# Kernel tuning notes

Hardware: AMD Instinct MI355X
Metric: run time of the kernel (lower is better)

The kernel has to match this reference:

```python
import jax, jax.numpy as jnp
import numpy as np

N_NODES = 50000
N_EDGES = 800000
IN_F = 128
HID = 128
N_REL = 8


def setup_inputs() -> dict:
    key = jax.random.key(0)
    ks = jax.random.split(key, 12)
    s = 0.05
    return {
        "in_feat": jax.random.normal(ks[0], (N_NODES, IN_F), dtype=jnp.float32),
        "W1": jax.random.normal(ks[1], (N_REL, IN_F, HID), dtype=jnp.float32) * s,
        "W1_self": jax.random.normal(ks[2], (IN_F, HID), dtype=jnp.float32) * s,
        "b1": jnp.zeros((HID,), dtype=jnp.float32),
        "W2": jax.random.normal(ks[3], (N_REL, HID, HID), dtype=jnp.float32) * s,
        "W2_self": jax.random.normal(ks[4], (HID, HID), dtype=jnp.float32) * s,
        "b2": jnp.zeros((HID,), dtype=jnp.float32),
        "fc_w": jax.random.normal(ks[5], (HID, 1), dtype=jnp.float32) * s,
        "fc_b": jnp.zeros((1,), dtype=jnp.float32),
        "src": jax.random.randint(ks[6], (N_EDGES,), 0, N_NODES),
        "dst": jax.random.randint(ks[7], (N_EDGES,), 0, N_NODES),
        "etypes": jax.random.randint(ks[8], (N_EDGES,), 0, N_REL),
    }


def _rel_graph_conv(h, W, W_self, b, src, dst, etypes, n_nodes):
    # Transform node features once per relation: [R, N, H]
    xr = jnp.einsum('nd,rdh->rnh', h, W)
    # Per-edge message: gather relation-specific transformed source features [E, H]
    msgs = xr[etypes, src]
    # Scatter-sum aggregation to destination nodes [N, H]
    agg = jax.ops.segment_sum(msgs, dst, num_segments=n_nodes)
    # Self-loop + bias + ReLU (DGL RelGraphConv defaults)
    return jax.nn.relu(agg + h @ W_self + b)


def reference(in_feat, W1, W1_self, b1, W2, W2_self, b2, fc_w, fc_b, src, dst, etypes):
    n = in_feat.shape[0]
    h = _rel_graph_conv(in_feat, W1, W1_self, b1, src, dst, etypes, n)
    # dropout layers are identity in eval mode
    h = _rel_graph_conv(h, W2, W2_self, b2, src, dst, etypes, n)
    pooled = jnp.mean(h, axis=0, keepdims=True)  # AvgPooling over one graph -> [1, H]
    logits = pooled @ fc_w + fc_b                # [1, 1]
    return jax.nn.sigmoid(logits)
```

## Files before the change

kernel.cpp:

```cpp
#include <hip/hip_runtime.h>

#define NNODES 50000
#define NEDGES 800000
#define F 128
#define NREL 8
#define NOUT 1152
#define NBKT 98
#define BSH 9
#define SEG 16384
#define NTILES 391
#define GEMM_BLOCKS (8 * 9 * 49)
#define CSR_BLOCKS 196

typedef float f32x4 __attribute__((ext_vector_type(4)));
typedef float f32x2 __attribute__((ext_vector_type(2)));

typedef __attribute__((address_space(3))) void lds_void;
typedef const __attribute__((address_space(1))) void glb_void;
__device__ __forceinline__ void gll16(const void* g, void* l) {
  __builtin_amdgcn_global_load_lds(
      (glb_void*)(unsigned long long)g,
      (lds_void*)(unsigned)(unsigned long long)l, 16, 0, 0);
}

#define PREP_ZERO  33
#define PREP_CVT   6250
#define PREP_W     144
__global__ __launch_bounds__(256)
void k_prep(const float* __restrict__ in_feat, unsigned* __restrict__ feat0,
            const float* __restrict__ W1, const float* __restrict__ W1s,
            unsigned* __restrict__ Wt1,
            const float* __restrict__ W2, const float* __restrict__ W2s,
            unsigned* __restrict__ Wt2,
            float* __restrict__ pooled_p, int* __restrict__ bcur) {
  const int b = blockIdx.x, t = threadIdx.x;
  if (b < 32) {
    pooled_p[b * 256 + t] = 0.f;
  } else if (b < PREP_ZERO) {
    if (t <= NBKT) bcur[t] = 0;
  } else if (b < PREP_ZERO + PREP_CVT) {
    int i = (b - PREP_ZERO) * 256 + t;
    float4 v = ((const float4*)in_feat)[i];
    unsigned pk = 0;
    pk = __builtin_amdgcn_cvt_pk_fp8_f32(v.x, v.y, pk, false);
    pk = __builtin_amdgcn_cvt_pk_fp8_f32(v.z, v.w, pk, true);
    feat0[i] = pk;
  } else {
    int w2 = (b >= PREP_ZERO + PREP_CVT + PREP_W);
    int idx = (b - PREP_ZERO - PREP_CVT - (w2 ? PREP_W : 0)) * 256 + t;
    int n = idx >> 5, k0 = (idx & 31) * 4;
    int r = n >> 7, c = n & 127;
    const float* Wr = w2 ? W2 : W1;
    const float* Ws = w2 ? W2s : W1s;
    float v0, v1, v2, v3;
    if (r < NREL) {
      v0 = Wr[((size_t)(r * F + k0 + 0)) * F + c];
      v1 = Wr[((size_t)(r * F + k0 + 1)) * F + c];
      v2 = Wr[((size_t)(r * F + k0 + 2)) * F + c];
      v3 = Wr[((size_t)(r * F + k0 + 3)) * F + c];
    } else {
      v0 = Ws[(size_t)(k0 + 0) * F + c];
      v1 = Ws[(size_t)(k0 + 1) * F + c];
      v2 = Ws[(size_t)(k0 + 2) * F + c];
      v3 = Ws[(size_t)(k0 + 3) * F + c];
    }
    unsigned pk = 0;
    pk = __builtin_amdgcn_cvt_pk_fp8_f32(v0, v1, pk, false);
    pk = __builtin_amdgcn_cvt_pk_fp8_f32(v2, v3, pk, true);
    (w2 ? Wt2 : Wt1)[idx] = pk;
  }
}

__global__ __launch_bounds__(512)
void k_fsort(const int* __restrict__ ebuf, const int* __restrict__ bcur,
             int* __restrict__ rowptr, int* __restrict__ edata) {
  __shared__ int cnt[512];
  __shared__ int pos[512];
  __shared__ int ws2[512];
  __shared__ int bc_s;
  const int b = blockIdx.x, t = threadIdx.x;
  int myc = (t < NBKT) ? bcur[t] : 0;
  ws2[t] = (t < b) ? myc : 0;
  if (t == b) bc_s = myc;
  __syncthreads();
  for (int off = 1; off < 512; off <<= 1) {
    int x = (t >= off) ? ws2[t - off] : 0;
    __syncthreads();
    ws2[t] += x;
    __syncthreads();
  }
  const int beg = ws2[511];
  const int cntb = bc_s;
  const int sbeg = b * SEG;

  cnt[t] = 0;
  __syncthreads();
  for (int e = t; e < cntb; e += 512)
    atomicAdd(&cnt[((unsigned)ebuf[sbeg + e]) >> 19], 1);
  __syncthreads();
  int myn = cnt[t];
  ws2[t] = myn;
  __syncthreads();
  for (int off = 1; off < 512; off <<= 1) {
    int x = (t >= off) ? ws2[t - off] : 0;
    __syncthreads();
    ws2[t] += x;
    __syncthreads();
  }
  pos[t] = ws2[t] - myn;
  __syncthreads();
  int node = (b << BSH) + t;
  if (node < NNODES) rowptr[node] = beg + pos[t];
  if (b == NBKT - 1 && t == 0) rowptr[NNODES] = NEDGES;
  __syncthreads();
  for (int e = t; e < cntb; e += 512) {
    int rec = ebuf[sbeg + e];
    int c = ((unsigned)rec) >> 19;
    int lrank = atomicAdd(&pos[c], 1);
    int srcv = (rec >> 3) & 0xFFFF;
    int etv = rec & 7;
    edata[beg + lrank] = srcv * NOUT + etv * F;
  }
}

__global__ __launch_bounds__(512, 8)
void gemm_xrs(const unsigned char* __restrict__ A,
              const unsigned char* __restrict__ Wt,
              unsigned char* __restrict__ xrs, int doCsr,
              const int* __restrict__ src, const int* __restrict__ dst,
              const int* __restrict__ et, int* __restrict__ bcur,
              int* __restrict__ ebuf) {
  __shared__ uint4 As[1024];
  __shared__ uint4 Bs[1024];
  __shared__ int lhist[NBKT];
  __shared__ int lbase[NBKT];
  const int tid = threadIdx.x;

  if (doCsr && blockIdx.x < CSR_BLOCKS) {
    if (tid < NBKT) lhist[tid] = 0;
    __syncthreads();
    int e0 = blockIdx.x * 4096;
    int rec[8], cc[8], lr[8];
#pragma unroll
    for (int i = 0; i < 8; ++i) {
      int e = e0 + tid + i * 512;
      if (e < NEDGES) {
        int d = dst[e];
        cc[i] = d >> BSH;
        rec[i] = ((d & 511) << 19) | (src[e] << 3) | et[e];
        lr[i] = atomicAdd(&lhist[cc[i]], 1);
      } else {
        cc[i] = -1;
      }
    }
    __syncthreads();
    if (tid < NBKT && lhist[tid] > 0) lbase[tid] = atomicAdd(&bcur[tid], lhist[tid]);
    __syncthreads();
#pragma unroll
    for (int i = 0; i < 8; ++i)
      if (cc[i] >= 0) ebuf[cc[i] * SEG + lbase[cc[i]] + lr[i]] = rec[i];
    return;
  }

  const int id = blockIdx.x - (doCsr ? CSR_BLOCKS : 0);
  const int x = id & 7, j = id >> 3;
  const int tile = (j / 9) * 8 + x;
  const int cb = j % 9;
  if (tile >= NTILES) return;
  const int row0 = tile * 128;

  const int lane = tid & 63;
  const int w = tid >> 6;
  const int i16 = lane & 15, q = lane >> 4;
  const int mbase = (w & 3) * 32, nbase = (w >> 2) * 64;

#pragma unroll
  for (int i = 0; i < 2; ++i) {
    int L = tid + i * 512;
    int r = L >> 3, c8s = L & 7;
    int c8 = c8s ^ (r & 7);
    int agr = row0 + r; if (agr >= NNODES) agr = NNODES - 1;
    gll16((const void*)(A + (size_t)agr * F + c8 * 16), (void*)&As[L]);
    gll16((const void*)(Wt + ((size_t)cb * 128 + r) * F + c8 * 16), (void*)&Bs[L]);
  }
  __syncthreads();

  f32x4 acc[2][4];
#pragma unroll
  for (int a = 0; a < 2; ++a)
#pragma unroll
    for (int b = 0; b < 4; ++b) acc[a][b] = (f32x4)0.f;

  const char* Ab = (const char*)As;
  const char* Bb = (const char*)Bs;
#pragma unroll
  for (int c = 0; c < 4; ++c) {
    const int ch = c * 2 + (q >> 1);
    const int h8 = (q & 1) << 3;
    long af[2], bfr[4];
#pragma unroll
    for (int mi = 0; mi < 2; ++mi) {
      int r = mbase + mi * 16 + i16;
      af[mi] = *(const long*)(Ab + r * 128 + ((ch ^ (r & 7)) << 4) + h8);
    }
#pragma unroll
    for (int ni = 0; ni < 4; ++ni) {
      int r = nbase + ni * 16 + i16;
      bfr[ni] = *(const long*)(Bb + r * 128 + ((ch ^ (r & 7)) << 4) + h8);
    }
#pragma unroll
    for (int mi = 0; mi < 2; ++mi)
#pragma unroll
      for (int ni = 0; ni < 4; ++ni)
        acc[mi][ni] = __builtin_amdgcn_mfma_f32_16x16x32_fp8_fp8(
            bfr[ni], af[mi], acc[mi][ni], 0, 0, 0);
  }

  unsigned pkv[2][4];
#pragma unroll
  for (int mi = 0; mi < 2; ++mi)
#pragma unroll
    for (int ni = 0; ni < 4; ++ni) {
      f32x4 v = acc[mi][ni];
      unsigned pk = 0;
      pk = __builtin_amdgcn_cvt_pk_fp8_f32(v[0], v[1], pk, false);
      pk = __builtin_amdgcn_cvt_pk_fp8_f32(v[2], v[3], pk, true);
      pkv[mi][ni] = pk;
    }

  __syncthreads();
  unsigned* sbuf = (unsigned*)As;
  {
    const int dbase = (nbase >> 2) + q;
#pragma unroll
    for (int mi = 0; mi < 2; ++mi) {
      int nl = mbase + mi * 16 + i16;
      int sw = (nl & 7) << 2;
      int vb_ = nl * 32;
#pragma unroll
      for (int ni = 0; ni < 4; ++ni)
        sbuf[vb_ + ((dbase + ni * 4) ^ sw)] = pkv[mi][ni];
    }
  }
  __syncthreads();

#pragma unroll
  for (int k = 0; k < 2; ++k) {
    int nl = k * 64 + (tid >> 3);
    int ch = tid & 7;
    int d0 = (ch * 4) ^ ((nl & 7) << 2);
    uint4 v = *(const uint4*)&sbuf[nl * 32 + d0];
    int row = row0 + nl;
    if (row < NNODES)
      *(uint4*)(xrs + (size_t)row * NOUT + cb * 128 + ch * 16) = v;
  }
}

__global__ __launch_bounds__(256)
void k_aggregate(const unsigned char* __restrict__ xrs,
                 const int* __restrict__ rowptr, const int* __restrict__ edata,
                 const float* __restrict__ bias, unsigned char* __restrict__ hout,
                 float* __restrict__ pooled_p) {
  __shared__ float red[16][128];
  const int wv = threadIdx.x >> 6;
  const int lane = threadIdx.x & 63;
  const int G = lane >> 4, s = lane & 15;
  const int node = blockIdx.x * 16 + wv * 4 + G;
  const int beg = rowptr[node], end = rowptr[node + 1];

  float a[8];
#pragma unroll
  for (int j = 0; j < 8; ++j) a[j] = 0.f;

  {
    uint2 sv = *(const uint2*)(xrs + (size_t)node * NOUT + NREL * F + s * 8);
    f32x2 l0 = __builtin_amdgcn_cvt_pk_f32_fp8(sv.x, false);
    f32x2 h0 = __builtin_amdgcn_cvt_pk_f32_fp8(sv.x, true);
    f32x2 l1 = __builtin_amdgcn_cvt_pk_f32_fp8(sv.y, false);
    f32x2 h1 = __builtin_amdgcn_cvt_pk_f32_fp8(sv.y, true);
    a[0] += l0[0]; a[1] += l0[1]; a[2] += h0[0]; a[3] += h0[1];
    a[4] += l1[0]; a[5] += l1[1]; a[6] += h1[0]; a[7] += h1[1];
  }

  for (int base = beg; base < end; base += 16) {
    int cnt = end - base; if (cnt > 16) cnt = 16;
    int my = (base + s < end) ? edata[base + s] : 0;
    uint2 v[16];
#pragma unroll
    for (int k = 0; k < 16; ++k) {
      if (k < cnt) {
        int off = __shfl(my, k, 16);
        v[k] = *(const uint2*)(xrs + (size_t)off + s * 8);
      }
    }
#pragma unroll
    for (int k = 0; k < 16; ++k) {
      if (k < cnt) {
        f32x2 l0 = __builtin_amdgcn_cvt_pk_f32_fp8(v[k].x, false);
        f32x2 h0 = __builtin_amdgcn_cvt_pk_f32_fp8(v[k].x, true);
        f32x2 l1 = __builtin_amdgcn_cvt_pk_f32_fp8(v[k].y, false);
        f32x2 h1 = __builtin_amdgcn_cvt_pk_f32_fp8(v[k].y, true);
        a[0] += l0[0]; a[1] += l0[1]; a[2] += h0[0]; a[3] += h0[1];
        a[4] += l1[0]; a[5] += l1[1]; a[6] += h1[0]; a[7] += h1[1];
      }
    }
  }

  float4 bb0 = ((const float4*)bias)[s * 2];
  float4 bb1 = ((const float4*)bias)[s * 2 + 1];
  a[0] = fmaxf(a[0] + bb0.x, 0.f);
  a[1] = fmaxf(a[1] + bb0.y, 0.f);
  a[2] = fmaxf(a[2] + bb0.z, 0.f);
  a[3] = fmaxf(a[3] + bb0.w, 0.f);
  a[4] = fmaxf(a[4] + bb1.x, 0.f);
  a[5] = fmaxf(a[5] + bb1.y, 0.f);
  a[6] = fmaxf(a[6] + bb1.z, 0.f);
  a[7] = fmaxf(a[7] + bb1.w, 0.f);

  if (hout) {
    uint2 pk;
    unsigned p0 = 0;
    p0 = __builtin_amdgcn_cvt_pk_fp8_f32(a[0], a[1], p0, false);
    p0 = __builtin_amdgcn_cvt_pk_fp8_f32(a[2], a[3], p0, true);
    unsigned p1 = 0;
    p1 = __builtin_amdgcn_cvt_pk_fp8_f32(a[4], a[5], p1, false);
    p1 = __builtin_amdgcn_cvt_pk_fp8_f32(a[6], a[7], p1, true);
    pk.x = p0; pk.y = p1;
    ((uint2*)(hout + (size_t)node * F))[s] = pk;
  } else {
#pragma unroll
    for (int j = 0; j < 8; ++j) red[wv * 4 + G][s * 8 + j] = a[j];
    __syncthreads();
    if (threadIdx.x < 128) {
      float sm = 0.f;
#pragma unroll
      for (int r = 0; r < 16; ++r) sm += red[r][threadIdx.x];
      atomicAdd(&pooled_p[(blockIdx.x & 63) * 128 + threadIdx.x], sm);
    }
  }
}

__global__ __launch_bounds__(128)
void k_final(const float* __restrict__ pooled_p, const float* __restrict__ fcw,
             const float* __restrict__ fcb, float* __restrict__ out) {
  __shared__ float s[128];
  int t = threadIdx.x;
  float acc = 0.f;
#pragma unroll 8
  for (int k = 0; k < 64; ++k) acc += pooled_p[k * 128 + t];
  s[t] = acc * (1.0f / (float)NNODES) * fcw[t];
  __syncthreads();
  if (t == 0) {
    float v = 0.f;
    for (int i = 0; i < 128; ++i) v += s[i];
    v += fcb[0];
    out[0] = 1.f / (1.f + expf(-v));
  }
}

extern "C" void kernel_launch(void* const* d_in, const int* in_sizes, int n_in,
                              void* d_out, int out_size, void* d_ws, size_t ws_size,
                              hipStream_t stream) {
  const float* in_feat = (const float*)d_in[0];
  const float* W1      = (const float*)d_in[1];
  const float* W1s     = (const float*)d_in[2];
  const float* b1      = (const float*)d_in[3];
  const float* W2      = (const float*)d_in[4];
  const float* W2s     = (const float*)d_in[5];
  const float* b2      = (const float*)d_in[6];
  const float* fcw     = (const float*)d_in[7];
  const float* fcb     = (const float*)d_in[8];
  const int*   src     = (const int*)d_in[9];
  const int*   dst     = (const int*)d_in[10];
  const int*   et      = (const int*)d_in[11];
  float* out = (float*)d_out;

  unsigned char* xrs = (unsigned char*)d_ws;
  unsigned char* feat0 = xrs + (size_t)NNODES * NOUT;
  unsigned char* h1  = feat0 + (size_t)NNODES * F;
  unsigned char* Wt1 = h1 + (size_t)NNODES * F;
  unsigned char* Wt2 = Wt1 + (size_t)NOUT * F;
  float* pooled_p = (float*)(Wt2 + (size_t)NOUT * F);
  int*   bcur   = (int*)(pooled_p + 64 * 128);
  int*   rowptr = bcur + NBKT + 1;
  int*   ebuf   = rowptr + NNODES + 2;
  int*   edata  = ebuf + NBKT * SEG;

  k_prep<<<PREP_ZERO + PREP_CVT + 2 * PREP_W, 256, 0, stream>>>(
      in_feat, (unsigned*)feat0, W1, W1s, (unsigned*)Wt1,
      W2, W2s, (unsigned*)Wt2, pooled_p, bcur);

  const int aggBlocks = NNODES / 16;

  gemm_xrs<<<CSR_BLOCKS + GEMM_BLOCKS, 512, 0, stream>>>(
      feat0, Wt1, xrs, 1, src, dst, et, bcur, ebuf);
  k_fsort<<<NBKT, 512, 0, stream>>>(ebuf, bcur, rowptr, edata);
  k_aggregate<<<aggBlocks, 256, 0, stream>>>(xrs, rowptr, edata, b1, h1, nullptr);
  gemm_xrs<<<GEMM_BLOCKS, 512, 0, stream>>>(
      h1, Wt2, xrs, 0, src, dst, et, bcur, ebuf);
  k_aggregate<<<aggBlocks, 256, 0, stream>>>(xrs, rowptr, edata, b2, nullptr, pooled_p);

  k_final<<<1, 128, 0, stream>>>(pooled_p, fcw, fcb, out);
}
```

Before: 207.1 us.

## Aggregate raw features per relation before GEMM instead of transforming then gathering

The layer order changes from transform-then-aggregate to aggregate-then-transform. Edges are sorted by destination and relation, each node's neighbour features are summed per relation into a 1152-wide fp8 row (8 relations plus self), and one K=1152 GEMM then applies bias and ReLU, with the pooling reduction fused into the second layer's GEMM epilogue. Gathers now read 128-byte source rows instead of rows of the large per-relation transformed buffer. The CSR build moves into the prep kernel, and a memset replaces the zeroing blocks. In exchange, the per-relation partial sums are rounded to fp8, which adds precision loss, and the GEMM now has a longer K loop with no load/compute overlap.

```diff
diff --git a/kernel.cpp b/kernel.cpp
--- a/kernel.cpp
+++ b/kernel.cpp
@@ -8,8 +8,7 @@
 #define NBKT 98
 #define BSH 9
 #define SEG 16384
-#define NTILES 391
-#define GEMM_BLOCKS (8 * 9 * 49)
+#define NT64 782
 #define CSR_BLOCKS 196
 
 typedef float f32x4 __attribute__((ext_vector_type(4)));
@@ -23,7 +22,6 @@
       (lds_void*)(unsigned)(unsigned long long)l, 16, 0, 0);
 }
 
-#define PREP_ZERO  33
 #define PREP_CVT   6250
 #define PREP_W     144
 __global__ __launch_bounds__(256)
@@ -32,118 +30,20 @@
             unsigned* __restrict__ Wt1,
             const float* __restrict__ W2, const float* __restrict__ W2s,
             unsigned* __restrict__ Wt2,
-            float* __restrict__ pooled_p, int* __restrict__ bcur) {
+            const int* __restrict__ src, const int* __restrict__ dst,
+            const int* __restrict__ et,
+            int* __restrict__ bcur, int* __restrict__ ebuf) {
   const int b = blockIdx.x, t = threadIdx.x;
-  if (b < 32) {
-    pooled_p[b * 256 + t] = 0.f;
-  } else if (b < PREP_ZERO) {
-    if (t <= NBKT) bcur[t] = 0;
-  } else if (b < PREP_ZERO + PREP_CVT) {
-    int i = (b - PREP_ZERO) * 256 + t;
-    float4 v = ((const float4*)in_feat)[i];
-    unsigned pk = 0;
-    pk = __builtin_amdgcn_cvt_pk_fp8_f32(v.x, v.y, pk, false);
-    pk = __builtin_amdgcn_cvt_pk_fp8_f32(v.z, v.w, pk, true);
-    feat0[i] = pk;
-  } else {
-    int w2 = (b >= PREP_ZERO + PREP_CVT + PREP_W);
-    int idx = (b - PREP_ZERO - PREP_CVT - (w2 ? PREP_W : 0)) * 256 + t;
-    int n = idx >> 5, k0 = (idx & 31) * 4;
-    int r = n >> 7, c = n & 127;
-    const float* Wr = w2 ? W2 : W1;
-    const float* Ws = w2 ? W2s : W1s;
-    float v0, v1, v2, v3;
-    if (r < NREL) {
-      v0 = Wr[((size_t)(r * F + k0 + 0)) * F + c];
-      v1 = Wr[((size_t)(r * F + k0 + 1)) * F + c];
-      v2 = Wr[((size_t)(r * F + k0 + 2)) * F + c];
-      v3 = Wr[((size_t)(r * F + k0 + 3)) * F + c];
-    } else {
-      v0 = Ws[(size_t)(k0 + 0) * F + c];
-      v1 = Ws[(size_t)(k0 + 1) * F + c];
-      v2 = Ws[(size_t)(k0 + 2) * F + c];
-      v3 = Ws[(size_t)(k0 + 3) * F + c];
-    }
-    unsigned pk = 0;
-    pk = __builtin_amdgcn_cvt_pk_fp8_f32(v0, v1, pk, false);
-    pk = __builtin_amdgcn_cvt_pk_fp8_f32(v2, v3, pk, true);
-    (w2 ? Wt2 : Wt1)[idx] = pk;
-  }
-}
-
-__global__ __launch_bounds__(512)
-void k_fsort(const int* __restrict__ ebuf, const int* __restrict__ bcur,
-             int* __restrict__ rowptr, int* __restrict__ edata) {
-  __shared__ int cnt[512];
-  __shared__ int pos[512];
-  __shared__ int ws2[512];
-  __shared__ int bc_s;
-  const int b = blockIdx.x, t = threadIdx.x;
-  int myc = (t < NBKT) ? bcur[t] : 0;
-  ws2[t] = (t < b) ? myc : 0;
-  if (t == b) bc_s = myc;
-  __syncthreads();
-  for (int off = 1; off < 512; off <<= 1) {
-    int x = (t >= off) ? ws2[t - off] : 0;
-    __syncthreads();
-    ws2[t] += x;
-    __syncthreads();
-  }
-  const int beg = ws2[511];
-  const int cntb = bc_s;
-  const int sbeg = b * SEG;
-
-  cnt[t] = 0;
-  __syncthreads();
-  for (int e = t; e < cntb; e += 512)
-    atomicAdd(&cnt[((unsigned)ebuf[sbeg + e]) >> 19], 1);
-  __syncthreads();
-  int myn = cnt[t];
-  ws2[t] = myn;
-  __syncthreads();
-  for (int off = 1; off < 512; off <<= 1) {
-    int x = (t >= off) ? ws2[t - off] : 0;
-    __syncthreads();
-    ws2[t] += x;
-    __syncthreads();
-  }
-  pos[t] = ws2[t] - myn;
-  __syncthreads();
-  int node = (b << BSH) + t;
-  if (node < NNODES) rowptr[node] = beg + pos[t];
-  if (b == NBKT - 1 && t == 0) rowptr[NNODES] = NEDGES;
-  __syncthreads();
-  for (int e = t; e < cntb; e += 512) {
-    int rec = ebuf[sbeg + e];
-    int c = ((unsigned)rec) >> 19;
-    int lrank = atomicAdd(&pos[c], 1);
-    int srcv = (rec >> 3) & 0xFFFF;
-    int etv = rec & 7;
-    edata[beg + lrank] = srcv * NOUT + etv * F;
-  }
-}
-
-__global__ __launch_bounds__(512, 8)
-void gemm_xrs(const unsigned char* __restrict__ A,
-              const unsigned char* __restrict__ Wt,
-              unsigned char* __restrict__ xrs, int doCsr,
-              const int* __restrict__ src, const int* __restrict__ dst,
-              const int* __restrict__ et, int* __restrict__ bcur,
-              int* __restrict__ ebuf) {
-  __shared__ uint4 As[1024];
-  __shared__ uint4 Bs[1024];
-  __shared__ int lhist[NBKT];
-  __shared__ int lbase[NBKT];
-  const int tid = threadIdx.x;
-
-  if (doCsr && blockIdx.x < CSR_BLOCKS) {
-    if (tid < NBKT) lhist[tid] = 0;
-    __syncthreads();
-    int e0 = blockIdx.x * 4096;
-    int rec[8], cc[8], lr[8];
-#pragma unroll
-    for (int i = 0; i < 8; ++i) {
-      int e = e0 + tid + i * 512;
+  if (b < CSR_BLOCKS) {
+    __shared__ int lhist[NBKT];
+    __shared__ int lbase[NBKT];
+    if (t < NBKT) lhist[t] = 0;
+    __syncthreads();
+    int e0 = b * 4096;
+    int rec[16], cc[16], lr[16];
+#pragma unroll
+    for (int i = 0; i < 16; ++i) {
+      int e = e0 + t + i * 256;
       if (e < NEDGES) {
         int d = dst[e];
         cc[i] = d >> BSH;
@@ -154,36 +54,169 @@
       }
     }
     __syncthreads();
-    if (tid < NBKT && lhist[tid] > 0) lbase[tid] = atomicAdd(&bcur[tid], lhist[tid]);
-    __syncthreads();
-#pragma unroll
-    for (int i = 0; i < 8; ++i)
+    if (t < NBKT && lhist[t] > 0) lbase[t] = atomicAdd(&bcur[t], lhist[t]);
+    __syncthreads();
+#pragma unroll
+    for (int i = 0; i < 16; ++i)
       if (cc[i] >= 0) ebuf[cc[i] * SEG + lbase[cc[i]] + lr[i]] = rec[i];
-    return;
-  }
-
-  const int id = blockIdx.x - (doCsr ? CSR_BLOCKS : 0);
-  const int x = id & 7, j = id >> 3;
-  const int tile = (j / 9) * 8 + x;
-  const int cb = j % 9;
-  if (tile >= NTILES) return;
-  const int row0 = tile * 128;
-
+  } else if (b < CSR_BLOCKS + PREP_CVT) {
+    int i = (b - CSR_BLOCKS) * 256 + t;
+    float4 v = ((const float4*)in_feat)[i];
+    unsigned pk = 0;
+    pk = __builtin_amdgcn_cvt_pk_fp8_f32(v.x, v.y, pk, false);
+    pk = __builtin_amdgcn_cvt_pk_fp8_f32(v.z, v.w, pk, true);
+    feat0[i] = pk;
+  } else {
+    int rem = b - CSR_BLOCKS - PREP_CVT;
+    int w2 = rem >= PREP_W;
+    int idx = (rem - (w2 ? PREP_W : 0)) * 256 + t;
+    int c = idx / 288, u = idx - c * 288;
+    int k0 = u * 4, r = k0 >> 7, kk = k0 & 127;
+    const float* Wr = w2 ? W2 : W1;
+    const float* Ws = w2 ? W2s : W1s;
+    float v0, v1, v2, v3;
+    if (r < NREL) {
+      v0 = Wr[r * 16384 + (kk + 0) * 128 + c];
+      v1 = Wr[r * 16384 + (kk + 1) * 128 + c];
+      v2 = Wr[r * 16384 + (kk + 2) * 128 + c];
+      v3 = Wr[r * 16384 + (kk + 3) * 128 + c];
+    } else {
+      v0 = Ws[(kk + 0) * 128 + c];
+      v1 = Ws[(kk + 1) * 128 + c];
+      v2 = Ws[(kk + 2) * 128 + c];
+      v3 = Ws[(kk + 3) * 128 + c];
+    }
+    unsigned pk = 0;
+    pk = __builtin_amdgcn_cvt_pk_fp8_f32(v0, v1, pk, false);
+    pk = __builtin_amdgcn_cvt_pk_fp8_f32(v2, v3, pk, true);
+    (w2 ? Wt2 : Wt1)[idx] = pk;
+  }
+}
+
+__global__ __launch_bounds__(512)
+void k_fsort(const int* __restrict__ ebuf, const int* __restrict__ bcur,
+             int* __restrict__ rowptr2, int* __restrict__ edata) {
+  __shared__ int cnt[4096];
+  __shared__ int pos4[4096];
+  __shared__ int ws2[512];
+  __shared__ int bc_s;
+  const int b = blockIdx.x, t = threadIdx.x;
+  int myc = (t < NBKT) ? bcur[t] : 0;
+  ws2[t] = (t < b) ? myc : 0;
+  if (t == b) bc_s = myc;
+  __syncthreads();
+  for (int off = 1; off < 512; off <<= 1) {
+    int x = (t >= off) ? ws2[t - off] : 0;
+    __syncthreads();
+    ws2[t] += x;
+    __syncthreads();
+  }
+  const int beg = ws2[511];
+  const int cntb = bc_s;
+  const int sbeg = b * SEG;
+
+#pragma unroll
+  for (int i = 0; i < 8; ++i) cnt[t * 8 + i] = 0;
+  __syncthreads();
+  for (int e = t; e < cntb; e += 512) {
+    int rec = ebuf[sbeg + e];
+    int key = ((((unsigned)rec) >> 19) << 3) | (rec & 7);
+    atomicAdd(&cnt[key], 1);
+  }
+  __syncthreads();
+  int loc[8]; int tot = 0;
+#pragma unroll
+  for (int i = 0; i < 8; ++i) { loc[i] = tot; tot += cnt[t * 8 + i]; }
+  ws2[t] = tot;
+  __syncthreads();
+  for (int off = 1; off < 512; off <<= 1) {
+    int x = (t >= off) ? ws2[t - off] : 0;
+    __syncthreads();
+    ws2[t] += x;
+    __syncthreads();
+  }
+  int base = beg + ws2[t] - tot;
+#pragma unroll
+  for (int i = 0; i < 8; ++i) pos4[t * 8 + i] = base + loc[i];
+  __syncthreads();
+#pragma unroll
+  for (int i = 0; i < 8; ++i)
+    rowptr2[b * 4096 + t * 8 + i] = pos4[t * 8 + i];
+  __syncthreads();
+  for (int e = t; e < cntb; e += 512) {
+    int rec = ebuf[sbeg + e];
+    int key = ((((unsigned)rec) >> 19) << 3) | (rec & 7);
+    int p = atomicAdd(&pos4[key], 1);
+    edata[p] = (rec >> 3) & 0xFFFF;
+  }
+}
+
+__global__ __launch_bounds__(256)
+void k_aggf(const unsigned char* __restrict__ feat,
+            const int* __restrict__ rowptr2, const int* __restrict__ edata,
+            unsigned char* __restrict__ agg) {
+  const int lane = threadIdx.x & 63;
+  const int wv = threadIdx.x >> 6;
+  const int G = lane >> 4, s = lane & 15;
+  const int node = blockIdx.x * 16 + wv * 4 + G;
+
+  int rp = (s <= 8) ? rowptr2[node * 8 + s] : 0;
+  uint2 fv = *(const uint2*)(feat + (size_t)node * F + s * 8);
+  *(uint2*)(agg + (size_t)node * NOUT + NREL * F + s * 8) = fv;
+
+#pragma unroll
+  for (int r = 0; r < NREL; ++r) {
+    int beg = __shfl(rp, r, 16);
+    int end = __shfl(rp, r + 1, 16);
+    float a[8];
+#pragma unroll
+    for (int j = 0; j < 8; ++j) a[j] = 0.f;
+    for (int base = beg; base < end; base += 16) {
+      int cn = end - base; if (cn > 16) cn = 16;
+      int my = (base + s < end) ? edata[base + s] : 0;
+      uint2 v[16];
+#pragma unroll
+      for (int k = 0; k < 16; ++k) {
+        if (k < cn) {
+          int off = __shfl(my, k, 16);
+          v[k] = *(const uint2*)(feat + (size_t)off * F + s * 8);
+        }
+      }
+#pragma unroll
+      for (int k = 0; k < 16; ++k) {
+        if (k < cn) {
+          f32x2 l0 = __builtin_amdgcn_cvt_pk_f32_fp8(v[k].x, false);
+          f32x2 h0 = __builtin_amdgcn_cvt_pk_f32_fp8(v[k].x, true);
+          f32x2 l1 = __builtin_amdgcn_cvt_pk_f32_fp8(v[k].y, false);
+          f32x2 h1 = __builtin_amdgcn_cvt_pk_f32_fp8(v[k].y, true);
+          a[0] += l0[0]; a[1] += l0[1]; a[2] += h0[0]; a[3] += h0[1];
+          a[4] += l1[0]; a[5] += l1[1]; a[6] += h1[0]; a[7] += h1[1];
+        }
+      }
+    }
+    unsigned p0 = 0, p1 = 0;
+    p0 = __builtin_amdgcn_cvt_pk_fp8_f32(a[0], a[1], p0, false);
+    p0 = __builtin_amdgcn_cvt_pk_fp8_f32(a[2], a[3], p0, true);
+    p1 = __builtin_amdgcn_cvt_pk_fp8_f32(a[4], a[5], p1, false);
+    p1 = __builtin_amdgcn_cvt_pk_fp8_f32(a[6], a[7], p1, true);
+    uint2 pk; pk.x = p0; pk.y = p1;
+    *(uint2*)(agg + (size_t)node * NOUT + r * F + s * 8) = pk;
+  }
+}
+
+__global__ __launch_bounds__(256)
+void k_gemm(const unsigned char* __restrict__ A,
+            const unsigned char* __restrict__ Wt,
+            const float* __restrict__ bias, unsigned char* __restrict__ hout,
+            float* __restrict__ pooled_p) {
+  __shared__ uint4 As[512];
+  __shared__ uint4 Bs[1024];
+  const int tid = threadIdx.x;
+  const int row0 = blockIdx.x * 64;
   const int lane = tid & 63;
   const int w = tid >> 6;
   const int i16 = lane & 15, q = lane >> 4;
-  const int mbase = (w & 3) * 32, nbase = (w >> 2) * 64;
-
-#pragma unroll
-  for (int i = 0; i < 2; ++i) {
-    int L = tid + i * 512;
-    int r = L >> 3, c8s = L & 7;
-    int c8 = c8s ^ (r & 7);
-    int agr = row0 + r; if (agr >= NNODES) agr = NNODES - 1;
-    gll16((const void*)(A + (size_t)agr * F + c8 * 16), (void*)&As[L]);
-    gll16((const void*)(Wt + ((size_t)cb * 128 + r) * F + c8 * 16), (void*)&Bs[L]);
-  }
-  __syncthreads();
+  const int mbase = (w & 1) * 32, nbase = (w >> 1) * 64;
 
   f32x4 acc[2][4];
 #pragma unroll
@@ -193,45 +226,72 @@
 
   const char* Ab = (const char*)As;
   const char* Bb = (const char*)Bs;
-#pragma unroll
-  for (int c = 0; c < 4; ++c) {
-    const int ch = c * 2 + (q >> 1);
-    const int h8 = (q & 1) << 3;
-    long af[2], bfr[4];
-#pragma unroll
-    for (int mi = 0; mi < 2; ++mi) {
-      int r = mbase + mi * 16 + i16;
-      af[mi] = *(const long*)(Ab + r * 128 + ((ch ^ (r & 7)) << 4) + h8);
-    }
-#pragma unroll
-    for (int ni = 0; ni < 4; ++ni) {
-      int r = nbase + ni * 16 + i16;
-      bfr[ni] = *(const long*)(Bb + r * 128 + ((ch ^ (r & 7)) << 4) + h8);
-    }
+
+  for (int kc = 0; kc < 9; ++kc) {
+#pragma unroll
+    for (int i = 0; i < 2; ++i) {
+      int L = tid + i * 256;
+      int r = L >> 3, c8s = L & 7;
+      int c8 = c8s ^ (r & 7);
+      int agr = row0 + r; if (agr >= NNODES) agr = NNODES - 1;
+      gll16((const void*)(A + (size_t)agr * NOUT + kc * 128 + c8 * 16),
+            (void*)&As[L]);
+    }
+#pragma unroll
+    for (int i = 0; i < 4; ++i) {
+      int L = tid + i * 256;
+      int r = L >> 3, c8s = L & 7;
+      int c8 = c8s ^ (r & 7);
+      gll16((const void*)(Wt + (size_t)r * NOUT + kc * 128 + c8 * 16),
+            (void*)&Bs[L]);
+    }
+    __syncthreads();
+
+#pragma unroll
+    for (int c = 0; c < 4; ++c) {
+      const int ch = c * 2 + (q >> 1);
+      const int h8 = (q & 1) << 3;
+      long af[2], bfr[4];
+#pragma unroll
+      for (int mi = 0; mi < 2; ++mi) {
+        int r = mbase + mi * 16 + i16;
+        af[mi] = *(const long*)(Ab + r * 128 + ((ch ^ (r & 7)) << 4) + h8);
+      }
+#pragma unroll
+      for (int ni = 0; ni < 4; ++ni) {
+        int r = nbase + ni * 16 + i16;
+        bfr[ni] = *(const long*)(Bb + r * 128 + ((ch ^ (r & 7)) << 4) + h8);
+      }
+#pragma unroll
+      for (int mi = 0; mi < 2; ++mi)
+#pragma unroll
+        for (int ni = 0; ni < 4; ++ni)
+          acc[mi][ni] = __builtin_amdgcn_mfma_f32_16x16x32_fp8_fp8(
+              bfr[ni], af[mi], acc[mi][ni], 0, 0, 0);
+    }
+    __syncthreads();
+  }
+
+  const int dbase = (nbase >> 2) + q;
+
+  if (hout) {
+    unsigned pkv[2][4];
 #pragma unroll
     for (int mi = 0; mi < 2; ++mi)
 #pragma unroll
-      for (int ni = 0; ni < 4; ++ni)
-        acc[mi][ni] = __builtin_amdgcn_mfma_f32_16x16x32_fp8_fp8(
-            bfr[ni], af[mi], acc[mi][ni], 0, 0, 0);
-  }
-
-  unsigned pkv[2][4];
-#pragma unroll
-  for (int mi = 0; mi < 2; ++mi)
-#pragma unroll
-    for (int ni = 0; ni < 4; ++ni) {
-      f32x4 v = acc[mi][ni];
-      unsigned pk = 0;
-      pk = __builtin_amdgcn_cvt_pk_fp8_f32(v[0], v[1], pk, false);
-      pk = __builtin_amdgcn_cvt_pk_fp8_f32(v[2], v[3], pk, true);
-      pkv[mi][ni] = pk;
-    }
-
-  __syncthreads();
-  unsigned* sbuf = (unsigned*)As;
-  {
-    const int dbase = (nbase >> 2) + q;
+      for (int ni = 0; ni < 4; ++ni) {
+        f32x4 v = acc[mi][ni];
+        float4 bb = ((const float4*)bias)[dbase + ni * 4];
+        float r0 = fmaxf(v[0] + bb.x, 0.f);
+        float r1 = fmaxf(v[1] + bb.y, 0.f);
+        float r2 = fmaxf(v[2] + bb.z, 0.f);
+        float r3 = fmaxf(v[3] + bb.w, 0.f);
+        unsigned pk = 0;
+        pk = __builtin_amdgcn_cvt_pk_fp8_f32(r0, r1, pk, false);
+        pk = __builtin_amdgcn_cvt_pk_fp8_f32(r2, r3, pk, true);
+        pkv[mi][ni] = pk;
+      }
+    unsigned* sbuf = (unsigned*)As;
 #pragma unroll
     for (int mi = 0; mi < 2; ++mi) {
       int nl = mbase + mi * 16 + i16;
@@ -241,101 +301,47 @@
       for (int ni = 0; ni < 4; ++ni)
         sbuf[vb_ + ((dbase + ni * 4) ^ sw)] = pkv[mi][ni];
     }
-  }
-  __syncthreads();
-
-#pragma unroll
-  for (int k = 0; k < 2; ++k) {
-    int nl = k * 64 + (tid >> 3);
-    int ch = tid & 7;
-    int d0 = (ch * 4) ^ ((nl & 7) << 2);
-    uint4 v = *(const uint4*)&sbuf[nl * 32 + d0];
-    int row = row0 + nl;
-    if (row < NNODES)
-      *(uint4*)(xrs + (size_t)row * NOUT + cb * 128 + ch * 16) = v;
-  }
-}
-
-__global__ __launch_bounds__(256)
-void k_aggregate(const unsigned char* __restrict__ xrs,
-                 const int* __restrict__ rowptr, const int* __restrict__ edata,
-                 const float* __restrict__ bias, unsigned char* __restrict__ hout,
-                 float* __restrict__ pooled_p) {
-  __shared__ float red[16][128];
-  const int wv = threadIdx.x >> 6;
-  const int lane = threadIdx.x & 63;
-  const int G = lane >> 4, s = lane & 15;
-  const int node = blockIdx.x * 16 + wv * 4 + G;
-  const int beg = rowptr[node], end = rowptr[node + 1];
-
-  float a[8];
-#pragma unroll
-  for (int j = 0; j < 8; ++j) a[j] = 0.f;
-
-  {
-    uint2 sv = *(const uint2*)(xrs + (size_t)node * NOUT + NREL * F + s * 8);
-    f32x2 l0 = __builtin_amdgcn_cvt_pk_f32_fp8(sv.x, false);
-    f32x2 h0 = __builtin_amdgcn_cvt_pk_f32_fp8(sv.x, true);
-    f32x2 l1 = __builtin_amdgcn_cvt_pk_f32_fp8(sv.y, false);
-    f32x2 h1 = __builtin_amdgcn_cvt_pk_f32_fp8(sv.y, true);
-    a[0] += l0[0]; a[1] += l0[1]; a[2] += h0[0]; a[3] += h0[1];
-    a[4] += l1[0]; a[5] += l1[1]; a[6] += h1[0]; a[7] += h1[1];
-  }
-
-  for (int base = beg; base < end; base += 16) {
-    int cnt = end - base; if (cnt > 16) cnt = 16;
-    int my = (base + s < end) ? edata[base + s] : 0;
-    uint2 v[16];
-#pragma unroll
-    for (int k = 0; k < 16; ++k) {
-      if (k < cnt) {
-        int off = __shfl(my, k, 16);
-        v[k] = *(const uint2*)(xrs + (size_t)off + s * 8);
-      }
-    }
-#pragma unroll
-    for (int k = 0; k < 16; ++k) {
-      if (k < cnt) {
-        f32x2 l0 = __builtin_amdgcn_cvt_pk_f32_fp8(v[k].x, false);
-        f32x2 h0 = __builtin_amdgcn_cvt_pk_f32_fp8(v[k].x, true);
-        f32x2 l1 = __builtin_amdgcn_cvt_pk_f32_fp8(v[k].y, false);
-        f32x2 h1 = __builtin_amdgcn_cvt_pk_f32_fp8(v[k].y, true);
-        a[0] += l0[0]; a[1] += l0[1]; a[2] += h0[0]; a[3] += h0[1];
-        a[4] += l1[0]; a[5] += l1[1]; a[6] += h1[0]; a[7] += h1[1];
-      }
-    }
-  }
-
-  float4 bb0 = ((const float4*)bias)[s * 2];
-  float4 bb1 = ((const float4*)bias)[s * 2 + 1];
-  a[0] = fmaxf(a[0] + bb0.x, 0.f);
-  a[1] = fmaxf(a[1] + bb0.y, 0.f);
-  a[2] = fmaxf(a[2] + bb0.z, 0.f);
-  a[3] = fmaxf(a[3] + bb0.w, 0.f);
-  a[4] = fmaxf(a[4] + bb1.x, 0.f);
-  a[5] = fmaxf(a[5] + bb1.y, 0.f);
-  a[6] = fmaxf(a[6] + bb1.z, 0.f);
-  a[7] = fmaxf(a[7] + bb1.w, 0.f);
-
-  if (hout) {
-    uint2 pk;
-    unsigned p0 = 0;
-    p0 = __builtin_amdgcn_cvt_pk_fp8_f32(a[0], a[1], p0, false);
-    p0 = __builtin_amdgcn_cvt_pk_fp8_f32(a[2], a[3], p0, true);
-    unsigned p1 = 0;
-    p1 = __builtin_amdgcn_cvt_pk_fp8_f32(a[4], a[5], p1, false);
-    p1 = __builtin_amdgcn_cvt_pk_fp8_f32(a[6], a[7], p1, true);
-    pk.x = p0; pk.y = p1;
-    ((uint2*)(hout + (size_t)node * F))[s] = pk;
+    __syncthreads();
+#pragma unroll
+    for (int k = 0; k < 2; ++k) {
+      int nl = k * 32 + (tid >> 3);
+      int ch = tid & 7;
+      int d0 = (ch * 4) ^ ((nl & 7) << 2);
+      uint4 v = *(const uint4*)&sbuf[nl * 32 + d0];
+      int row = row0 + nl;
+      if (row < NNODES)
+        *(uint4*)(hout + (size_t)row * F + ch * 16) = v;
+    }
   } else {
 #pragma unroll
-    for (int j = 0; j < 8; ++j) red[wv * 4 + G][s * 8 + j] = a[j];
-    __syncthreads();
-    if (threadIdx.x < 128) {
-      float sm = 0.f;
-#pragma unroll
-      for (int r = 0; r < 16; ++r) sm += red[r][threadIdx.x];
-      atomicAdd(&pooled_p[(blockIdx.x & 63) * 128 + threadIdx.x], sm);
+    for (int ni = 0; ni < 4; ++ni) {
+      float4 bb = ((const float4*)bias)[dbase + ni * 4];
+      float t4[4];
+#pragma unroll
+      for (int j = 0; j < 4; ++j) t4[j] = 0.f;
+#pragma unroll
+      for (int mi = 0; mi < 2; ++mi) {
+        int row = row0 + mbase + mi * 16 + i16;
+        bool ok = row < NNODES;
+        f32x4 v = acc[mi][ni];
+        t4[0] += ok ? fmaxf(v[0] + bb.x, 0.f) : 0.f;
+        t4[1] += ok ? fmaxf(v[1] + bb.y, 0.f) : 0.f;
+        t4[2] += ok ? fmaxf(v[2] + bb.z, 0.f) : 0.f;
+        t4[3] += ok ? fmaxf(v[3] + bb.w, 0.f) : 0.f;
+      }
+#pragma unroll
+      for (int j = 0; j < 4; ++j) {
+        t4[j] += __shfl_xor(t4[j], 1, 64);
+        t4[j] += __shfl_xor(t4[j], 2, 64);
+        t4[j] += __shfl_xor(t4[j], 4, 64);
+        t4[j] += __shfl_xor(t4[j], 8, 64);
+      }
+      if (i16 == 0) {
+        int out0 = (dbase + ni * 4) * 4;
+#pragma unroll
+        for (int j = 0; j < 4; ++j)
+          atomicAdd(&pooled_p[(blockIdx.x & 63) * 128 + out0 + j], t4[j]);
+      }
     }
   }
 }
@@ -375,30 +381,28 @@
   const int*   et      = (const int*)d_in[11];
   float* out = (float*)d_out;
 
-  unsigned char* xrs = (unsigned char*)d_ws;
-  unsigned char* feat0 = xrs + (size_t)NNODES * NOUT;
-  unsigned char* h1  = feat0 + (size_t)NNODES * F;
-  unsigned char* Wt1 = h1 + (size_t)NNODES * F;
-  unsigned char* Wt2 = Wt1 + (size_t)NOUT * F;
-  float* pooled_p = (float*)(Wt2 + (size_t)NOUT * F);
-  int*   bcur   = (int*)(pooled_p + 64 * 128);
-  int*   rowptr = bcur + NBKT + 1;
-  int*   ebuf   = rowptr + NNODES + 2;
-  int*   edata  = ebuf + NBKT * SEG;
-
-  k_prep<<<PREP_ZERO + PREP_CVT + 2 * PREP_W, 256, 0, stream>>>(
-      in_feat, (unsigned*)feat0, W1, W1s, (unsigned*)Wt1,
-      W2, W2s, (unsigned*)Wt2, pooled_p, bcur);
-
-  const int aggBlocks = NNODES / 16;
-
-  gemm_xrs<<<CSR_BLOCKS + GEMM_BLOCKS, 512, 0, stream>>>(
-      feat0, Wt1, xrs, 1, src, dst, et, bcur, ebuf);
-  k_fsort<<<NBKT, 512, 0, stream>>>(ebuf, bcur, rowptr, edata);
-  k_aggregate<<<aggBlocks, 256, 0, stream>>>(xrs, rowptr, edata, b1, h1, nullptr);
-  gemm_xrs<<<GEMM_BLOCKS, 512, 0, stream>>>(
-      h1, Wt2, xrs, 0, src, dst, et, bcur, ebuf);
-  k_aggregate<<<aggBlocks, 256, 0, stream>>>(xrs, rowptr, edata, b2, nullptr, pooled_p);
+  unsigned char* agg  = (unsigned char*)d_ws;
+  unsigned char* feat0 = agg + (size_t)NNODES * NOUT;
+  unsigned char* h1   = feat0 + (size_t)NNODES * F;
+  unsigned char* Wtp1 = h1 + (size_t)NNODES * F;
+  unsigned char* Wtp2 = Wtp1 + (size_t)128 * NOUT;
+  float* pooled_p = (float*)(Wtp2 + (size_t)128 * NOUT);
+  int*   bcur    = (int*)(pooled_p + 64 * 128);
+  int*   rowptr2 = bcur + NBKT + 1;
+  int*   ebuf    = rowptr2 + NBKT * 4096;
+  int*   edata   = ebuf + NBKT * SEG;
+
+  hipMemsetAsync(pooled_p, 0, (64 * 128 + NBKT + 1) * sizeof(float), stream);
+
+  k_prep<<<CSR_BLOCKS + PREP_CVT + 2 * PREP_W, 256, 0, stream>>>(
+      in_feat, (unsigned*)feat0, W1, W1s, (unsigned*)Wtp1,
+      W2, W2s, (unsigned*)Wtp2, src, dst, et, bcur, ebuf);
+  k_fsort<<<NBKT, 512, 0, stream>>>(ebuf, bcur, rowptr2, edata);
+
+  k_aggf<<<NNODES / 16, 256, 0, stream>>>(feat0, rowptr2, edata, agg);
+  k_gemm<<<NT64, 256, 0, stream>>>(agg, Wtp1, b1, h1, nullptr);
+  k_aggf<<<NNODES / 16, 256, 0, stream>>>(h1, rowptr2, edata, agg);
+  k_gemm<<<NT64, 256, 0, stream>>>(agg, Wtp2, b2, nullptr, pooled_p);
 
   k_final<<<1, 128, 0, stream>>>(pooled_p, fcw, fcb, out);
 }
```

New measurement: 266.0 us. +28.4%, slower.
